# Optimization experiments

Measured on AMD Instinct MI355X. Metric: run time of the kernel, lower is better.

Reference implementation:

```python
import jax, jax.numpy as jnp
import numpy as np

B, L, V, E, H, K, T = 256, 49, 10000, 512, 512, 512, 15


def setup_inputs() -> dict:
    key = jax.random.key(0)
    ks = jax.random.split(key, 16)
    s = 0.02
    return {
        "features": jax.random.normal(ks[0], (B, L, K), dtype=jnp.float32),
        "captions": jax.random.randint(ks[1], (B, T), 0, V),
        "emb": jax.random.normal(ks[2], (V, E), dtype=jnp.float32) * s,
        "Wq": jax.random.normal(ks[3], (H, H), dtype=jnp.float32) * s,
        "bq": jnp.zeros((H,), jnp.float32),
        "Uk": jax.random.normal(ks[4], (H, K), dtype=jnp.float32) * s,
        "bk": jnp.zeros((H,), jnp.float32),
        "Va": jax.random.normal(ks[5], (1, H), dtype=jnp.float32) * s,
        "bva": jnp.zeros((1,), jnp.float32),
        "W0": jax.random.normal(ks[6], (H, K), dtype=jnp.float32) * s,
        "b0": jnp.zeros((H,), jnp.float32),
        "Wih": jax.random.normal(ks[7], (3 * H, E + H), dtype=jnp.float32) * s,
        "bih": jnp.zeros((3 * H,), jnp.float32),
        "Whh": jax.random.normal(ks[8], (3 * H, H), dtype=jnp.float32) * s,
        "bhh": jnp.zeros((3 * H,), jnp.float32),
        "W1": jax.random.normal(ks[9], (V, H), dtype=jnp.float32) * s,
        "b1": jnp.zeros((V,), jnp.float32),
    }


def reference(features, captions, emb, Wq, bq, Uk, bk, Va, bva, W0, b0, Wih, bih, Whh, bhh, W1, b1):
    # embeddings: [B, T, E]
    embeddings = emb[captions]
    # precompute key projection for additive attention: [B, L, H]
    keys_proj = jnp.einsum("blk,hk->blh", features, Uk) + bk

    def step(h, emb_t):  # h: [B,H], emb_t: [B,E]
        q = h @ Wq.T + bq                                  # [B, H]
        scores = jnp.tanh(q[:, None, :] + keys_proj) @ Va.T + bva  # [B, L, 1]
        w = jax.nn.softmax(scores, axis=1)                 # [B, L, 1]
        ctx = jnp.sum(w * features, axis=1)                # [B, K]
        ctx = ctx @ W0.T + b0                              # [B, H]
        x = jnp.concatenate([emb_t, ctx], axis=-1)         # [B, E+H]
        gi = x @ Wih.T + bih                               # [B, 3H]
        gh = h @ Whh.T + bhh                               # [B, 3H]
        i_r, i_z, i_n = jnp.split(gi, 3, axis=-1)
        h_r, h_z, h_n = jnp.split(gh, 3, axis=-1)
        r = jax.nn.sigmoid(i_r + h_r)
        z = jax.nn.sigmoid(i_z + h_z)
        n = jnp.tanh(i_n + r * h_n)
        h_new = (1.0 - z) * n + z * h
        out = h_new @ W1.T + b1                            # [B, V]
        return h_new, out

    h0 = jnp.zeros((features.shape[0], H), features.dtype)
    _, outs = jax.lax.scan(step, h0, jnp.swapaxes(embeddings, 0, 1))  # [T, B, V]
    return jnp.swapaxes(outs, 0, 1)  # [B, T, V]
```

## Files before the change

### kernel.cpp

```cpp
#include <hip/hip_runtime.h>
#include <hip/hip_bf16.h>
#include <math.h>

#define B_ 256
#define L_ 49
#define V_ 10000
#define E_ 512
#define H_ 512
#define K_ 512
#define T_ 15

typedef __bf16 bf16x8 __attribute__((ext_vector_type(8)));
typedef float f32x4 __attribute__((ext_vector_type(4)));

#define AS1 __attribute__((address_space(1)))
#define AS3 __attribute__((address_space(3)))

__device__ __forceinline__ float tanh_fast(float x)
{
    const float ax = fabsf(x);
    const float e = __expf(2.f * ax);
    const float t = 1.f - 2.f / (e + 1.f);
    return copysignf(t, x);
}

struct CvtSegs {
    const float* src[5];
    __hip_bfloat16* dst[5];
    int blk_end[5];
};

__global__ __launch_bounds__(256) void cvt_multi_kernel(CvtSegs s)
{
    const int blk = blockIdx.x;
    int seg = 0;
    while (blk >= s.blk_end[seg]) ++seg;
    const int base = seg ? s.blk_end[seg - 1] : 0;
    const int i = (blk - base) * 256 + threadIdx.x;
    const float4 v = ((const float4*)s.src[seg])[i];
    __hip_bfloat16 o[4];
    o[0] = (__hip_bfloat16)v.x; o[1] = (__hip_bfloat16)v.y;
    o[2] = (__hip_bfloat16)v.z; o[3] = (__hip_bfloat16)v.w;
    *(ushort4*)(s.dst[seg] + (size_t)i * 4) = *(ushort4*)o;
}

__global__ __launch_bounds__(256) void transpose_cast_kernel(
    const float* __restrict__ in, __hip_bfloat16* __restrict__ out, int R, int Cc)
{
    __shared__ float tile[32][33];
    const int tr0 = blockIdx.y * 32, tc0 = blockIdx.x * 32;
    const int tx = threadIdx.x & 31, ty = threadIdx.x >> 5;
#pragma unroll
    for (int i = 0; i < 32; i += 8)
        tile[ty + i][tx] = in[(size_t)(tr0 + ty + i) * Cc + tc0 + tx];
    __syncthreads();
#pragma unroll
    for (int i = 0; i < 32; i += 8)
        out[(size_t)(tc0 + ty + i) * R + tr0 + tx] = (__hip_bfloat16)tile[tx][ty + i];
}

__global__ __launch_bounds__(256) void bfull_kernel(
    const float* __restrict__ Wih, const float* __restrict__ b0,
    const float* __restrict__ bih, float* __restrict__ bfull)
{
    const int i = blockIdx.x * 256 + threadIdx.x;
    if (i >= 3 * H_) return;
    const float* wrow = Wih + (size_t)i * (E_ + H_) + E_;
    float acc = bih[i];
    for (int j = 0; j < H_; ++j) acc += wrow[j] * b0[j];
    bfull[i] = acc;
}

__global__ __launch_bounds__(128) void emb_gather_kernel(
    const int* __restrict__ caps, const float* __restrict__ emb,
    __hip_bfloat16* __restrict__ out)
{
    const int r = blockIdx.x;
    const int t = r >> 8;
    const int b = r & 255;
    const int cap = caps[(size_t)b * T_ + t];
    const int e = threadIdx.x * 4;
    const float4 v = *(const float4*)(emb + (size_t)cap * E_ + e);
    __hip_bfloat16 o[4];
    o[0] = (__hip_bfloat16)v.x; o[1] = (__hip_bfloat16)v.y;
    o[2] = (__hip_bfloat16)v.z; o[3] = (__hip_bfloat16)v.w;
    *(ushort4*)(out + (size_t)r * E_ + e) = *(ushort4*)o;
}

template <typename OutT>
__global__ __launch_bounds__(256) void gemm_bf16_nt128_kernel(
    const __hip_bfloat16* __restrict__ A, const __hip_bfloat16* __restrict__ Bw,
    const float* __restrict__ bias, OutT* __restrict__ C,
    int N, int Kd, int lda, int ldb, int ldc, int nby)
{
    int wg = blockIdx.x;
    {
        const int nwg = gridDim.x;
        const int q = nwg >> 3, r = nwg & 7;
        const int xcd = wg & 7, idx = wg >> 3;
        wg = (xcd < r ? xcd * (q + 1) : r * (q + 1) + (xcd - r) * q) + idx;
    }
    const int by = wg % nby;
    const int bx = wg / nby;
    const int row0 = by * 128;
    const int col0 = bx * 128;

    __shared__ __hip_bfloat16 Asl[128 * 64];
    __shared__ __hip_bfloat16 Bsl[128 * 64];
    const int tid  = threadIdx.x;
    const int lane = tid & 63;
    const int w    = tid >> 6;
    const int wm   = w >> 1, wn = w & 1;

    const int srow = tid >> 3;
    const int scol = (tid & 7) << 3;

    const int lr = lane & 15;
    const int lk = (lane >> 4) << 3;

    f32x4 acc[4][4] = {};

    const __hip_bfloat16* gA = A + (size_t)(row0 + srow) * lda + scol;
    bool bv[4];
    const __hip_bfloat16* gB[4];
#pragma unroll
    for (int i = 0; i < 4; ++i) {
        const int br = col0 + i * 32 + srow;
        bv[i] = br < N;
        gB[i] = Bw + (size_t)br * ldb + scol;
    }

    for (int k0 = 0; k0 < Kd; k0 += 64) {
        __syncthreads();
#pragma unroll
        for (int i = 0; i < 4; ++i)
            __builtin_amdgcn_global_load_lds((const AS1 void*)(gA + (size_t)i * 32 * lda + k0),
                (AS3 void*)(Asl + i * 2048 + tid * 8), 16, 0, 0);
#pragma unroll
        for (int i = 0; i < 4; ++i)
            if (bv[i]) __builtin_amdgcn_global_load_lds((const AS1 void*)(gB[i] + k0),
                (AS3 void*)(Bsl + i * 2048 + tid * 8), 16, 0, 0);
        __syncthreads();

#pragma unroll
        for (int ks = 0; ks < 2; ++ks) {
            bf16x8 af[4], bfr[4];
#pragma unroll
            for (int i = 0; i < 4; ++i)
                af[i] = *(const bf16x8*)(Asl + (wm * 64 + i * 16 + lr) * 64 + ks * 32 + lk);
#pragma unroll
            for (int j = 0; j < 4; ++j)
                bfr[j] = *(const bf16x8*)(Bsl + (wn * 64 + j * 16 + lr) * 64 + ks * 32 + lk);
#pragma unroll
            for (int i = 0; i < 4; ++i)
#pragma unroll
                for (int j = 0; j < 4; ++j)
                    acc[i][j] = __builtin_amdgcn_mfma_f32_16x16x32_bf16(
                        af[i], bfr[j], acc[i][j], 0, 0, 0);
        }
    }

    const int orow = (lane >> 4) << 2;
#pragma unroll
    for (int i = 0; i < 4; ++i) {
#pragma unroll
        for (int j = 0; j < 4; ++j) {
            const int col = col0 + wn * 64 + j * 16 + lr;
            if (col >= N) continue;
            const float bvv = bias ? bias[col] : 0.f;
            const int rowb = row0 + wm * 64 + i * 16 + orow;
#pragma unroll
            for (int r = 0; r < 4; ++r)
                C[(size_t)(rowb + r) * ldc + col] = (OutT)(acc[i][j][r] + bvv);
        }
    }
}

template <typename OutT>
__device__ __forceinline__ void gemm_nt_body(
    const __hip_bfloat16* __restrict__ A, const __hip_bfloat16* __restrict__ Bw,
    const float* __restrict__ bias, const float* __restrict__ Cin, int ldcin,
    OutT* __restrict__ C, int M, int N, int Kd, int lda, int ldb, int ldc,
    int bx, int by)
{
    __shared__ __hip_bfloat16 Asl[2][64 * 64];
    __shared__ __hip_bfloat16 Bsl[2][64 * 64];
    const int tid  = threadIdx.x;
    const int lane = tid & 63;
    const int w    = tid >> 6;
    const int wm   = w >> 1, wn = w & 1;
    const int row0 = by * 64;
    const int col0 = bx * 64;

    const int srow = tid >> 3;
    const int scol = (tid & 7) << 3;

    const int lr = lane & 15;
    const int lk = (lane >> 4) << 3;

    f32x4 acc[2][2] = {};

    const __hip_bfloat16* gA0 = A + (size_t)(row0 + srow) * lda + scol;
    const __hip_bfloat16* gA1 = gA0 + (size_t)32 * lda;
    const int br0 = col0 + srow, br1 = br0 + 32;
    const __hip_bfloat16* gB0 = Bw + (size_t)br0 * ldb + scol;
    const __hip_bfloat16* gB1 = gB0 + (size_t)32 * ldb;
    const bool v0 = br0 < N, v1 = br1 < N;

    auto stage = [&](int buf, int k0) {
        __builtin_amdgcn_global_load_lds((const AS1 void*)(gA0 + k0),
            (AS3 void*)(&Asl[buf][tid * 8]), 16, 0, 0);
        __builtin_amdgcn_global_load_lds((const AS1 void*)(gA1 + k0),
            (AS3 void*)(&Asl[buf][2048 + tid * 8]), 16, 0, 0);
        if (v0) __builtin_amdgcn_global_load_lds((const AS1 void*)(gB0 + k0),
            (AS3 void*)(&Bsl[buf][tid * 8]), 16, 0, 0);
        if (v1) __builtin_amdgcn_global_load_lds((const AS1 void*)(gB1 + k0),
            (AS3 void*)(&Bsl[buf][2048 + tid * 8]), 16, 0, 0);
    };

    stage(0, 0);
    __syncthreads();
    int cur = 0;
    for (int k0 = 0; k0 < Kd; k0 += 64) {
        if (k0 + 64 < Kd) stage(cur ^ 1, k0 + 64);

#pragma unroll
        for (int ks = 0; ks < 2; ++ks) {
            bf16x8 af[2], bfr[2];
#pragma unroll
            for (int i = 0; i < 2; ++i)
                af[i] = *(const bf16x8*)(&Asl[cur][(wm * 32 + i * 16 + lr) * 64 + ks * 32 + lk]);
#pragma unroll
            for (int j = 0; j < 2; ++j)
                bfr[j] = *(const bf16x8*)(&Bsl[cur][(wn * 32 + j * 16 + lr) * 64 + ks * 32 + lk]);
#pragma unroll
            for (int i = 0; i < 2; ++i)
#pragma unroll
                for (int j = 0; j < 2; ++j)
                    acc[i][j] = __builtin_amdgcn_mfma_f32_16x16x32_bf16(
                        af[i], bfr[j], acc[i][j], 0, 0, 0);
        }
        __syncthreads();
        cur ^= 1;
    }

    const int orow = (lane >> 4) << 2;
#pragma unroll
    for (int i = 0; i < 2; ++i) {
#pragma unroll
        for (int j = 0; j < 2; ++j) {
            const int col = col0 + wn * 32 + j * 16 + lr;
            if (col >= N) continue;
            const float bvv = bias ? bias[col] : 0.f;
            const int rowb = row0 + wm * 32 + i * 16 + orow;
#pragma unroll
            for (int r = 0; r < 4; ++r) {
                float v = acc[i][j][r] + bvv;
                if (Cin) v += Cin[(size_t)(rowb + r) * ldcin + col];
                C[(size_t)(rowb + r) * ldc + col] = (OutT)v;
            }
        }
    }
}

__global__ __launch_bounds__(256) void gemm_gigh_kernel(
    const __hip_bfloat16* __restrict__ ctx, const __hip_bfloat16* __restrict__ Wf,
    const float* __restrict__ gi_emb_t,
    const __hip_bfloat16* __restrict__ hb, const __hip_bfloat16* __restrict__ Whh,
    const float* __restrict__ bhh,
    float* __restrict__ gi, float* __restrict__ gh)
{
    if (blockIdx.z == 0)
        gemm_nt_body<float>(ctx, Wf, nullptr, gi_emb_t, 3 * H_, gi,
                            B_, 3 * H_, K_, K_, K_, 3 * H_, blockIdx.x, blockIdx.y);
    else
        gemm_nt_body<float>(hb, Whh, bhh, nullptr, 0, gh,
                            B_, 3 * H_, H_, H_, H_, 3 * H_, blockIdx.x, blockIdx.y);
}

__global__ __launch_bounds__(512) void attn_gru_kernel(
    const float* __restrict__ gi, const float* __restrict__ gh,
    float* __restrict__ h, __hip_bfloat16* __restrict__ hb,
    __hip_bfloat16* __restrict__ h_all, int tprev,
    const __hip_bfloat16* __restrict__ WqT, const float* __restrict__ bq,
    const __hip_bfloat16* __restrict__ kp, const __hip_bfloat16* __restrict__ feat,
    const float* __restrict__ Va, const float* __restrict__ bva,
    __hip_bfloat16* __restrict__ ctx)
{
    const int b = blockIdx.x;
    const int tid = threadIdx.x;
    const int lane = tid & 63;
    const int wave = tid >> 6;
    __shared__ float hb_s[H_];
    __shared__ float q_part[8][H_];
    __shared__ float q_s[H_];
    __shared__ float s_sc[64];
    __shared__ float s_w[64];

    if (tprev >= 0) {
        const int j = tid;
        const size_t o = (size_t)b * (3 * H_) + j;
        const float ir = gi[o],           hr = gh[o];
        const float iz = gi[o + H_],      hz = gh[o + H_];
        const float in_ = gi[o + 2 * H_], hn = gh[o + 2 * H_];
        const float rr = 1.f / (1.f + expf(-(ir + hr)));
        const float zz = 1.f / (1.f + expf(-(iz + hz)));
        const float nn = tanhf(in_ + rr * hn);
        const size_t hi = (size_t)b * H_ + j;
        const float hnew = (1.f - zz) * nn + zz * h[hi];
        h[hi] = hnew;
        hb_s[j] = hnew;
        const __hip_bfloat16 hv = (__hip_bfloat16)hnew;
        hb[hi] = hv;
        h_all[((size_t)b * T_ + tprev) * H_ + j] = hv;
    } else {
        hb_s[tid] = 0.f;
    }
    __syncthreads();

    {
        const int j0 = lane * 8;
        float accq[8] = {};
        const __hip_bfloat16* wbase = WqT + (size_t)(wave * 64) * H_ + j0;
#pragma unroll 16
        for (int k = 0; k < 64; ++k) {
            const float hv = hb_s[wave * 64 + k];
            const bf16x8 wv = *(const bf16x8*)(wbase + (size_t)k * H_);
#pragma unroll
            for (int i = 0; i < 8; ++i) accq[i] = fmaf(hv, (float)wv[i], accq[i]);
        }
#pragma unroll
        for (int i = 0; i < 8; ++i) q_part[wave][j0 + i] = accq[i];
    }
    __syncthreads();
    {
        const int j = tid;
        float s = bq[j];
#pragma unroll
        for (int w2 = 0; w2 < 8; ++w2) s += q_part[w2][j];
        q_s[j] = s;
    }
    __syncthreads();

    float qr[8], va[8];
#pragma unroll
    for (int i = 0; i < 8; ++i) {
        qr[i] = q_s[lane * 8 + i];
        va[i] = Va[lane * 8 + i];
    }

    for (int l = wave; l < L_; l += 8) {
        const bf16x8 kv = *(const bf16x8*)(kp + ((size_t)b * L_ + l) * H_ + lane * 8);
        float s = 0.f;
#pragma unroll
        for (int i = 0; i < 8; ++i) s += tanh_fast(qr[i] + (float)kv[i]) * va[i];
#pragma unroll
        for (int off = 32; off > 0; off >>= 1) s += __shfl_xor(s, off, 64);
        if (lane == 0) s_sc[l] = s + bva[0];
    }
    __syncthreads();

    if (wave == 0) {
        const float v = (lane < L_) ? s_sc[lane] : -1e30f;
        float m = v;
#pragma unroll
        for (int off = 32; off > 0; off >>= 1) m = fmaxf(m, __shfl_xor(m, off, 64));
        const float e = (lane < L_) ? expf(v - m) : 0.f;
        float ssum = e;
#pragma unroll
        for (int off = 32; off > 0; off >>= 1) ssum += __shfl_xor(ssum, off, 64);
        if (lane < L_) s_w[lane] = e / ssum;
    }
    __syncthreads();

    {
        float acc0 = 0.f;
        const __hip_bfloat16* fb = feat + (size_t)b * L_ * K_ + tid;
#pragma unroll 7
        for (int l = 0; l < L_; ++l)
            acc0 = fmaf(s_w[l], (float)fb[(size_t)l * K_], acc0);
        ctx[(size_t)b * K_ + tid] = (__hip_bfloat16)acc0;
    }
}

__global__ __launch_bounds__(256) void gru_kernel(
    const float* __restrict__ gi, const float* __restrict__ gh,
    float* __restrict__ h, __hip_bfloat16* __restrict__ hb,
    __hip_bfloat16* __restrict__ h_all, int t)
{
    const int idx = blockIdx.x * 256 + threadIdx.x;
    const int b = idx >> 9;
    const int j = idx & (H_ - 1);
    const size_t o = (size_t)b * 3 * H_ + j;
    const float ir = gi[o],           hr = gh[o];
    const float iz = gi[o + H_],      hz = gh[o + H_];
    const float in_ = gi[o + 2 * H_], hn = gh[o + 2 * H_];
    const float r = 1.f / (1.f + expf(-(ir + hr)));
    const float z = 1.f / (1.f + expf(-(iz + hz)));
    const float n = tanhf(in_ + r * hn);
    const float hnew = (1.f - z) * n + z * h[idx];
    h[idx] = hnew;
    const __hip_bfloat16 hv = (__hip_bfloat16)hnew;
    hb[idx] = hv;
    h_all[((size_t)b * T_ + t) * H_ + j] = hv;
}

extern "C" void kernel_launch(void* const* d_in, const int* in_sizes, int n_in,
                              void* d_out, int out_size, void* d_ws, size_t ws_size,
                              hipStream_t stream)
{
    const float* features = (const float*)d_in[0];
    const int*   captions = (const int*)d_in[1];
    const float* emb  = (const float*)d_in[2];
    const float* Wq   = (const float*)d_in[3];
    const float* bq   = (const float*)d_in[4];
    const float* Uk   = (const float*)d_in[5];
    const float* bk   = (const float*)d_in[6];
    const float* Va   = (const float*)d_in[7];
    const float* bva  = (const float*)d_in[8];
    const float* W0   = (const float*)d_in[9];
    const float* b0   = (const float*)d_in[10];
    const float* Wih  = (const float*)d_in[11];
    const float* bih  = (const float*)d_in[12];
    const float* Whh  = (const float*)d_in[13];
    const float* bhh  = (const float*)d_in[14];
    const float* W1   = (const float*)d_in[15];
    const float* b1   = (const float*)d_in[16];
    float* out = (float*)d_out;

    float* ws = (float*)d_ws;
    float* h      = ws; ws += B_ * H_;
    float* gi     = ws; ws += B_ * 3 * H_;
    float* gh     = ws; ws += B_ * 3 * H_;
    float* bfull  = ws; ws += 3 * H_;
    float* gi_emb = ws; ws += (size_t)T_ * B_ * 3 * H_;
    __hip_bfloat16* bws = (__hip_bfloat16*)ws;
    __hip_bfloat16* feat_bf = bws; bws += (size_t)B_ * L_ * K_;
    __hip_bfloat16* kp_bf   = bws; bws += (size_t)B_ * L_ * H_;
    __hip_bfloat16* W1_bf   = bws; bws += (size_t)V_ * H_;
    __hip_bfloat16* Uk_bf   = bws; bws += (size_t)H_ * K_;
    __hip_bfloat16* WqT_bf  = bws; bws += (size_t)H_ * H_;
    __hip_bfloat16* W0T_bf  = bws; bws += (size_t)K_ * H_;
    __hip_bfloat16* Wih_bf  = bws; bws += (size_t)3 * H_ * (E_ + H_);
    __hip_bfloat16* Whh_bf  = bws; bws += (size_t)3 * H_ * H_;
    __hip_bfloat16* Wfused  = bws; bws += (size_t)3 * H_ * K_;
    __hip_bfloat16* emb_all = bws; bws += (size_t)T_ * B_ * E_;
    __hip_bfloat16* hb      = bws; bws += (size_t)B_ * H_;
    __hip_bfloat16* ctx_bf  = bws; bws += (size_t)B_ * K_;
    __hip_bfloat16* h_all   = bws; bws += (size_t)B_ * T_ * H_;

    hipMemsetAsync(h, 0, (size_t)B_ * H_ * sizeof(float), stream);
    hipMemsetAsync(hb, 0, (size_t)B_ * H_ * sizeof(__hip_bfloat16), stream);

    const dim3 blk(256);

    {
        CvtSegs s;
        s.src[0] = features; s.dst[0] = feat_bf;
        s.src[1] = W1;       s.dst[1] = W1_bf;
        s.src[2] = Uk;       s.dst[2] = Uk_bf;
        s.src[3] = Wih;      s.dst[3] = Wih_bf;
        s.src[4] = Whh;      s.dst[4] = Whh_bf;
        const int nb[5] = {
            B_ * L_ * K_ / 1024, V_ * H_ / 1024, H_ * K_ / 1024,
            3 * H_ * (E_ + H_) / 1024, 3 * H_ * H_ / 1024 };
        int cum = 0;
        for (int i = 0; i < 5; ++i) { cum += nb[i]; s.blk_end[i] = cum; }
        cvt_multi_kernel<<<dim3(cum), blk, 0, stream>>>(s);
    }
    transpose_cast_kernel<<<dim3(H_ / 32, H_ / 32), blk, 0, stream>>>(Wq, WqT_bf, H_, H_);
    transpose_cast_kernel<<<dim3(K_ / 32, H_ / 32), blk, 0, stream>>>(W0, W0T_bf, H_, K_);
    bfull_kernel<<<dim3((3 * H_ + 255) / 256), blk, 0, stream>>>(Wih, b0, bih, bfull);
    emb_gather_kernel<<<dim3(T_ * B_), dim3(128), 0, stream>>>(captions, emb, emb_all);

    gemm_bf16_nt128_kernel<__hip_bfloat16><<<dim3((B_ * L_ / 128) * (H_ / 128)), blk, 0, stream>>>(
        feat_bf, Uk_bf, bk, kp_bf, H_, K_, K_, K_, H_, B_ * L_ / 128);

    gemm_bf16_nt128_kernel<__hip_bfloat16><<<dim3((3 * H_ / 128) * (K_ / 128)), blk, 0, stream>>>(
        Wih_bf + E_, W0T_bf, nullptr, Wfused, K_, H_, E_ + H_, H_, K_, 3 * H_ / 128);

    gemm_bf16_nt128_kernel<float><<<dim3((T_ * B_ / 128) * (3 * H_ / 128)), blk, 0, stream>>>(
        emb_all, Wih_bf, bfull, gi_emb, 3 * H_, E_, E_, E_ + H_, 3 * H_, T_ * B_ / 128);

    for (int t = 0; t < T_; ++t) {
        attn_gru_kernel<<<dim3(B_), dim3(512), 0, stream>>>(
            gi, gh, h, hb, h_all, t - 1,
            WqT_bf, bq, kp_bf, feat_bf, Va, bva, ctx_bf);
        gemm_gigh_kernel<<<dim3(3 * H_ / 64, B_ / 64, 2), blk, 0, stream>>>(
            ctx_bf, Wfused, gi_emb + (size_t)t * B_ * 3 * H_,
            hb, Whh_bf, bhh, gi, gh);
    }
    gru_kernel<<<dim3(B_ * H_ / 256), blk, 0, stream>>>(gi, gh, h, hb, h_all, T_ - 1);

    gemm_bf16_nt128_kernel<float><<<dim3((B_ * T_ / 128) * ((V_ + 127) / 128)), blk, 0, stream>>>(
        h_all, W1_bf, b1, out, V_, H_, H_, H_, V_, B_ * T_ / 128);
}
```

Measured before the change: 781.4 us.

## Use 128x128 tiles for per-step gate GEMMs, prefetch keys, fuse transposes

Replaces the double-buffered 64x64 GEMM body used for the per-step gi/gh gate GEMMs with the 128x128 single-buffered body, now with an optional residual-add input. The attention kernel preloads all key-projection rows into registers before the query computation so the loads overlap it. The two weight transpose-casts are merged into one launch. The larger tiles cut the per-step grid to 48 blocks, which raises per-block work and loses double buffering, at the risk of leaving most CUs idle.

```diff
diff --git a/kernel.cpp b/kernel.cpp
--- a/kernel.cpp
+++ b/kernel.cpp
@@ -44,9 +44,14 @@
     *(ushort4*)(s.dst[seg] + (size_t)i * 4) = *(ushort4*)o;
 }
 
-__global__ __launch_bounds__(256) void transpose_cast_kernel(
-    const float* __restrict__ in, __hip_bfloat16* __restrict__ out, int R, int Cc)
-{
+__global__ __launch_bounds__(256) void transpose_cast_dual_kernel(
+    const float* __restrict__ in0, __hip_bfloat16* __restrict__ out0,
+    const float* __restrict__ in1, __hip_bfloat16* __restrict__ out1)
+{
+    const float* in = blockIdx.z ? in1 : in0;
+    __hip_bfloat16* out = blockIdx.z ? out1 : out0;
+    const int R = H_;
+    const int Cc = blockIdx.z ? K_ : H_;
     __shared__ float tile[32][33];
     const int tr0 = blockIdx.y * 32, tc0 = blockIdx.x * 32;
     const int tx = threadIdx.x & 31, ty = threadIdx.x >> 5;
@@ -88,6 +93,90 @@
 }
 
 template <typename OutT>
+__device__ __forceinline__ void gemm_nt128_body(
+    const __hip_bfloat16* __restrict__ A, const __hip_bfloat16* __restrict__ Bw,
+    const float* __restrict__ bias, const float* __restrict__ Cin, int ldcin,
+    OutT* __restrict__ C, int N, int Kd, int lda, int ldb, int ldc,
+    int bx, int by)
+{
+    const int row0 = by * 128;
+    const int col0 = bx * 128;
+
+    __shared__ __hip_bfloat16 Asl[128 * 64];
+    __shared__ __hip_bfloat16 Bsl[128 * 64];
+    const int tid  = threadIdx.x;
+    const int lane = tid & 63;
+    const int w    = tid >> 6;
+    const int wm   = w >> 1, wn = w & 1;
+
+    const int srow = tid >> 3;
+    const int scol = (tid & 7) << 3;
+
+    const int lr = lane & 15;
+    const int lk = (lane >> 4) << 3;
+
+    f32x4 acc[4][4] = {};
+
+    const __hip_bfloat16* gA = A + (size_t)(row0 + srow) * lda + scol;
+    bool bv[4];
+    const __hip_bfloat16* gB[4];
+#pragma unroll
+    for (int i = 0; i < 4; ++i) {
+        const int br = col0 + i * 32 + srow;
+        bv[i] = br < N;
+        gB[i] = Bw + (size_t)br * ldb + scol;
+    }
+
+    for (int k0 = 0; k0 < Kd; k0 += 64) {
+        __syncthreads();
+#pragma unroll
+        for (int i = 0; i < 4; ++i)
+            __builtin_amdgcn_global_load_lds((const AS1 void*)(gA + (size_t)i * 32 * lda + k0),
+                (AS3 void*)(Asl + i * 2048 + tid * 8), 16, 0, 0);
+#pragma unroll
+        for (int i = 0; i < 4; ++i)
+            if (bv[i]) __builtin_amdgcn_global_load_lds((const AS1 void*)(gB[i] + k0),
+                (AS3 void*)(Bsl + i * 2048 + tid * 8), 16, 0, 0);
+        __syncthreads();
+
+#pragma unroll
+        for (int ks = 0; ks < 2; ++ks) {
+            bf16x8 af[4], bfr[4];
+#pragma unroll
+            for (int i = 0; i < 4; ++i)
+                af[i] = *(const bf16x8*)(Asl + (wm * 64 + i * 16 + lr) * 64 + ks * 32 + lk);
+#pragma unroll
+            for (int j = 0; j < 4; ++j)
+                bfr[j] = *(const bf16x8*)(Bsl + (wn * 64 + j * 16 + lr) * 64 + ks * 32 + lk);
+#pragma unroll
+            for (int i = 0; i < 4; ++i)
+#pragma unroll
+                for (int j = 0; j < 4; ++j)
+                    acc[i][j] = __builtin_amdgcn_mfma_f32_16x16x32_bf16(
+                        af[i], bfr[j], acc[i][j], 0, 0, 0);
+        }
+    }
+
+    const int orow = (lane >> 4) << 2;
+#pragma unroll
+    for (int i = 0; i < 4; ++i) {
+#pragma unroll
+        for (int j = 0; j < 4; ++j) {
+            const int col = col0 + wn * 64 + j * 16 + lr;
+            if (col >= N) continue;
+            const float bvv = bias ? bias[col] : 0.f;
+            const int rowb = row0 + wm * 64 + i * 16 + orow;
+#pragma unroll
+            for (int r = 0; r < 4; ++r) {
+                float v = acc[i][j][r] + bvv;
+                if (Cin) v += Cin[(size_t)(rowb + r) * ldcin + col];
+                C[(size_t)(rowb + r) * ldc + col] = (OutT)v;
+            }
+        }
+    }
+}
+
+template <typename OutT>
 __global__ __launch_bounds__(256) void gemm_bf16_nt128_kernel(
     const __hip_bfloat16* __restrict__ A, const __hip_bfloat16* __restrict__ Bw,
     const float* __restrict__ bias, OutT* __restrict__ C,
@@ -100,167 +189,8 @@
         const int xcd = wg & 7, idx = wg >> 3;
         wg = (xcd < r ? xcd * (q + 1) : r * (q + 1) + (xcd - r) * q) + idx;
     }
-    const int by = wg % nby;
-    const int bx = wg / nby;
-    const int row0 = by * 128;
-    const int col0 = bx * 128;
-
-    __shared__ __hip_bfloat16 Asl[128 * 64];
-    __shared__ __hip_bfloat16 Bsl[128 * 64];
-    const int tid  = threadIdx.x;
-    const int lane = tid & 63;
-    const int w    = tid >> 6;
-    const int wm   = w >> 1, wn = w & 1;
-
-    const int srow = tid >> 3;
-    const int scol = (tid & 7) << 3;
-
-    const int lr = lane & 15;
-    const int lk = (lane >> 4) << 3;
-
-    f32x4 acc[4][4] = {};
-
-    const __hip_bfloat16* gA = A + (size_t)(row0 + srow) * lda + scol;
-    bool bv[4];
-    const __hip_bfloat16* gB[4];
-#pragma unroll
-    for (int i = 0; i < 4; ++i) {
-        const int br = col0 + i * 32 + srow;
-        bv[i] = br < N;
-        gB[i] = Bw + (size_t)br * ldb + scol;
-    }
-
-    for (int k0 = 0; k0 < Kd; k0 += 64) {
-        __syncthreads();
-#pragma unroll
-        for (int i = 0; i < 4; ++i)
-            __builtin_amdgcn_global_load_lds((const AS1 void*)(gA + (size_t)i * 32 * lda + k0),
-                (AS3 void*)(Asl + i * 2048 + tid * 8), 16, 0, 0);
-#pragma unroll
-        for (int i = 0; i < 4; ++i)
-            if (bv[i]) __builtin_amdgcn_global_load_lds((const AS1 void*)(gB[i] + k0),
-                (AS3 void*)(Bsl + i * 2048 + tid * 8), 16, 0, 0);
-        __syncthreads();
-
-#pragma unroll
-        for (int ks = 0; ks < 2; ++ks) {
-            bf16x8 af[4], bfr[4];
-#pragma unroll
-            for (int i = 0; i < 4; ++i)
-                af[i] = *(const bf16x8*)(Asl + (wm * 64 + i * 16 + lr) * 64 + ks * 32 + lk);
-#pragma unroll
-            for (int j = 0; j < 4; ++j)
-                bfr[j] = *(const bf16x8*)(Bsl + (wn * 64 + j * 16 + lr) * 64 + ks * 32 + lk);
-#pragma unroll
-            for (int i = 0; i < 4; ++i)
-#pragma unroll
-                for (int j = 0; j < 4; ++j)
-                    acc[i][j] = __builtin_amdgcn_mfma_f32_16x16x32_bf16(
-                        af[i], bfr[j], acc[i][j], 0, 0, 0);
-        }
-    }
-
-    const int orow = (lane >> 4) << 2;
-#pragma unroll
-    for (int i = 0; i < 4; ++i) {
-#pragma unroll
-        for (int j = 0; j < 4; ++j) {
-            const int col = col0 + wn * 64 + j * 16 + lr;
-            if (col >= N) continue;
-            const float bvv = bias ? bias[col] : 0.f;
-            const int rowb = row0 + wm * 64 + i * 16 + orow;
-#pragma unroll
-            for (int r = 0; r < 4; ++r)
-                C[(size_t)(rowb + r) * ldc + col] = (OutT)(acc[i][j][r] + bvv);
-        }
-    }
-}
-
-template <typename OutT>
-__device__ __forceinline__ void gemm_nt_body(
-    const __hip_bfloat16* __restrict__ A, const __hip_bfloat16* __restrict__ Bw,
-    const float* __restrict__ bias, const float* __restrict__ Cin, int ldcin,
-    OutT* __restrict__ C, int M, int N, int Kd, int lda, int ldb, int ldc,
-    int bx, int by)
-{
-    __shared__ __hip_bfloat16 Asl[2][64 * 64];
-    __shared__ __hip_bfloat16 Bsl[2][64 * 64];
-    const int tid  = threadIdx.x;
-    const int lane = tid & 63;
-    const int w    = tid >> 6;
-    const int wm   = w >> 1, wn = w & 1;
-    const int row0 = by * 64;
-    const int col0 = bx * 64;
-
-    const int srow = tid >> 3;
-    const int scol = (tid & 7) << 3;
-
-    const int lr = lane & 15;
-    const int lk = (lane >> 4) << 3;
-
-    f32x4 acc[2][2] = {};
-
-    const __hip_bfloat16* gA0 = A + (size_t)(row0 + srow) * lda + scol;
-    const __hip_bfloat16* gA1 = gA0 + (size_t)32 * lda;
-    const int br0 = col0 + srow, br1 = br0 + 32;
-    const __hip_bfloat16* gB0 = Bw + (size_t)br0 * ldb + scol;
-    const __hip_bfloat16* gB1 = gB0 + (size_t)32 * ldb;
-    const bool v0 = br0 < N, v1 = br1 < N;
-
-    auto stage = [&](int buf, int k0) {
-        __builtin_amdgcn_global_load_lds((const AS1 void*)(gA0 + k0),
-            (AS3 void*)(&Asl[buf][tid * 8]), 16, 0, 0);
-        __builtin_amdgcn_global_load_lds((const AS1 void*)(gA1 + k0),
-            (AS3 void*)(&Asl[buf][2048 + tid * 8]), 16, 0, 0);
-        if (v0) __builtin_amdgcn_global_load_lds((const AS1 void*)(gB0 + k0),
-            (AS3 void*)(&Bsl[buf][tid * 8]), 16, 0, 0);
-        if (v1) __builtin_amdgcn_global_load_lds((const AS1 void*)(gB1 + k0),
-            (AS3 void*)(&Bsl[buf][2048 + tid * 8]), 16, 0, 0);
-    };
-
-    stage(0, 0);
-    __syncthreads();
-    int cur = 0;
-    for (int k0 = 0; k0 < Kd; k0 += 64) {
-        if (k0 + 64 < Kd) stage(cur ^ 1, k0 + 64);
-
-#pragma unroll
-        for (int ks = 0; ks < 2; ++ks) {
-            bf16x8 af[2], bfr[2];
-#pragma unroll
-            for (int i = 0; i < 2; ++i)
-                af[i] = *(const bf16x8*)(&Asl[cur][(wm * 32 + i * 16 + lr) * 64 + ks * 32 + lk]);
-#pragma unroll
-            for (int j = 0; j < 2; ++j)
-                bfr[j] = *(const bf16x8*)(&Bsl[cur][(wn * 32 + j * 16 + lr) * 64 + ks * 32 + lk]);
-#pragma unroll
-            for (int i = 0; i < 2; ++i)
-#pragma unroll
-                for (int j = 0; j < 2; ++j)
-                    acc[i][j] = __builtin_amdgcn_mfma_f32_16x16x32_bf16(
-                        af[i], bfr[j], acc[i][j], 0, 0, 0);
-        }
-        __syncthreads();
-        cur ^= 1;
-    }
-
-    const int orow = (lane >> 4) << 2;
-#pragma unroll
-    for (int i = 0; i < 2; ++i) {
-#pragma unroll
-        for (int j = 0; j < 2; ++j) {
-            const int col = col0 + wn * 32 + j * 16 + lr;
-            if (col >= N) continue;
-            const float bvv = bias ? bias[col] : 0.f;
-            const int rowb = row0 + wm * 32 + i * 16 + orow;
-#pragma unroll
-            for (int r = 0; r < 4; ++r) {
-                float v = acc[i][j][r] + bvv;
-                if (Cin) v += Cin[(size_t)(rowb + r) * ldcin + col];
-                C[(size_t)(rowb + r) * ldc + col] = (OutT)v;
-            }
-        }
-    }
+    gemm_nt128_body<OutT>(A, Bw, bias, nullptr, 0, C, N, Kd, lda, ldb, ldc,
+                          wg / nby, wg % nby);
 }
 
 __global__ __launch_bounds__(256) void gemm_gigh_kernel(
@@ -271,11 +201,11 @@
     float* __restrict__ gi, float* __restrict__ gh)
 {
     if (blockIdx.z == 0)
-        gemm_nt_body<float>(ctx, Wf, nullptr, gi_emb_t, 3 * H_, gi,
-                            B_, 3 * H_, K_, K_, K_, 3 * H_, blockIdx.x, blockIdx.y);
+        gemm_nt128_body<float>(ctx, Wf, nullptr, gi_emb_t, 3 * H_, gi,
+                               3 * H_, K_, K_, K_, 3 * H_, blockIdx.x, blockIdx.y);
     else
-        gemm_nt_body<float>(hb, Whh, bhh, nullptr, 0, gh,
-                            B_, 3 * H_, H_, H_, H_, 3 * H_, blockIdx.x, blockIdx.y);
+        gemm_nt128_body<float>(hb, Whh, bhh, nullptr, 0, gh,
+                               3 * H_, H_, H_, H_, 3 * H_, blockIdx.x, blockIdx.y);
 }
 
 __global__ __launch_bounds__(512) void attn_gru_kernel(
@@ -296,6 +226,14 @@
     __shared__ float q_s[H_];
     __shared__ float s_sc[64];
     __shared__ float s_w[64];
+
+    bf16x8 kpre[7];
+#pragma unroll
+    for (int i = 0; i < 7; ++i) {
+        const int l = wave + 8 * i;
+        if (l < L_)
+            kpre[i] = *(const bf16x8*)(kp + ((size_t)b * L_ + l) * H_ + lane * 8);
+    }
 
     if (tprev >= 0) {
         const int j = tid;
@@ -349,14 +287,18 @@
         va[i] = Va[lane * 8 + i];
     }
 
-    for (int l = wave; l < L_; l += 8) {
-        const bf16x8 kv = *(const bf16x8*)(kp + ((size_t)b * L_ + l) * H_ + lane * 8);
-        float s = 0.f;
-#pragma unroll
-        for (int i = 0; i < 8; ++i) s += tanh_fast(qr[i] + (float)kv[i]) * va[i];
-#pragma unroll
-        for (int off = 32; off > 0; off >>= 1) s += __shfl_xor(s, off, 64);
-        if (lane == 0) s_sc[l] = s + bva[0];
+#pragma unroll
+    for (int i = 0; i < 7; ++i) {
+        const int l = wave + 8 * i;
+        if (l < L_) {
+            float s = 0.f;
+#pragma unroll
+            for (int j = 0; j < 8; ++j)
+                s += tanh_fast(qr[j] + (float)kpre[i][j]) * va[j];
+#pragma unroll
+            for (int off = 32; off > 0; off >>= 1) s += __shfl_xor(s, off, 64);
+            if (lane == 0) s_sc[l] = s + bva[0];
+        }
     }
     __syncthreads();
 
@@ -468,8 +410,8 @@
         for (int i = 0; i < 5; ++i) { cum += nb[i]; s.blk_end[i] = cum; }
         cvt_multi_kernel<<<dim3(cum), blk, 0, stream>>>(s);
     }
-    transpose_cast_kernel<<<dim3(H_ / 32, H_ / 32), blk, 0, stream>>>(Wq, WqT_bf, H_, H_);
-    transpose_cast_kernel<<<dim3(K_ / 32, H_ / 32), blk, 0, stream>>>(W0, W0T_bf, H_, K_);
+    transpose_cast_dual_kernel<<<dim3(16, 16, 2), blk, 0, stream>>>(
+        Wq, WqT_bf, W0, W0T_bf);
     bfull_kernel<<<dim3((3 * H_ + 255) / 256), blk, 0, stream>>>(Wih, b0, bih, bfull);
     emb_gather_kernel<<<dim3(T_ * B_), dim3(128), 0, stream>>>(captions, emb, emb_all);
 
@@ -486,7 +428,7 @@
         attn_gru_kernel<<<dim3(B_), dim3(512), 0, stream>>>(
             gi, gh, h, hb, h_all, t - 1,
             WqT_bf, bq, kp_bf, feat_bf, Va, bva, ctx_bf);
-        gemm_gigh_kernel<<<dim3(3 * H_ / 64, B_ / 64, 2), blk, 0, stream>>>(
+        gemm_gigh_kernel<<<dim3(3 * H_ / 128, B_ / 128, 2), blk, 0, stream>>>(
             ctx_bf, Wfused, gi_emb + (size_t)t * B_ * 3 * H_,
             hb, Whh_bf, bhh, gi, gh);
     }
```

Result: slower. 1.021 ms (+30.7%).
